# Performance work log

Measured on AMD Instinct MI355X. Metric: run time of the kernel, lower is better.

Reference implementation:

```python
import jax, jax.numpy as jnp
import numpy as np

B, N, D = 1, 4096, 3072
H, DH = 16, 64
INNER = H * DH  # 1024
SCALE = DH ** -0.5
EPS = 1e-5


def setup_inputs() -> dict:
    key = jax.random.key(0)
    ks = jax.random.split(key, 4)
    x = jax.random.normal(ks[0], (B, N, D), jnp.float32)
    pe = jax.random.normal(ks[1], (1, 1, N, DH // 2, 2, 2), jnp.float32)
    w_qkv = jax.random.normal(ks[2], (3 * INNER, D), jnp.float32) * 0.02
    w_out = jax.random.normal(ks[3], (D, INNER), jnp.float32) * 0.02
    ln_g = jnp.ones((D,), jnp.float32)
    ln_b = jnp.zeros((D,), jnp.float32)
    return {"x": x, "pe": pe, "w_qkv": w_qkv, "w_out": w_out, "ln_g": ln_g, "ln_b": ln_b}


def _apply_rope(t, pe):
    # t: [b,h,n,d], pe: [1,1,n,d/2,2,2] (Flux rope layout)
    b, h, n, d = t.shape
    t_ = t.reshape(b, h, n, d // 2, 1, 2)
    out = pe[..., 0] * t_[..., 0] + pe[..., 1] * t_[..., 1]  # [b,h,n,d/2,2]
    return out.reshape(b, h, n, d)


def reference(x, pe, w_qkv, w_out, ln_g, ln_b):
    # LayerNorm (norm2)
    mu = jnp.mean(x, axis=-1, keepdims=True)
    var = jnp.mean((x - mu) ** 2, axis=-1, keepdims=True)
    xn = (x - mu) / jnp.sqrt(var + EPS) * ln_g + ln_b
    # QKV projection (no bias)
    qkv = xn @ w_qkv.T  # [b,n,3*inner]
    q, k, v = jnp.split(qkv, 3, axis=-1)
    def split_heads(t):
        return t.reshape(B, N, H, DH).transpose(0, 2, 1, 3)  # b h n d
    q, k, v = split_heads(q), split_heads(k), split_heads(v)
    # RoPE on q and k (attention_aug_bbox with mask=None, aug idx = -1 -> plain rope attn)
    q = _apply_rope(q, pe)
    k = _apply_rope(k, pe)
    scores = jnp.einsum('bhqd,bhkd->bhqk', q, k) * SCALE
    attn = jax.nn.softmax(scores, axis=-1)
    o = jnp.einsum('bhqk,bhkd->bhqd', attn, v)
    o = o.transpose(0, 2, 1, 3).reshape(B, N, INNER)  # b n (h d)
    return o @ w_out.T  # [b,n,dim]
```

## Files before the change

kernel.cpp:

```cpp
#include <hip/hip_runtime.h>
#include <hip/hip_bf16.h>

typedef unsigned short u16;
typedef __attribute__((ext_vector_type(8))) short bf16x8;
typedef __attribute__((ext_vector_type(4))) float f32x4;

#define N_TOK 4096
#define DMODEL 3072
#define NH 16
#define DHEAD 64
#define INNER 1024
#define SCALE_LOG2E 0.18033688011112042f

__device__ __forceinline__ u16 f2bf(float f) {
    union { float f; unsigned u; } un; un.f = f;
    unsigned r = un.u + 0x7fffu + ((un.u >> 16) & 1u);
    return (u16)(r >> 16);
}
__device__ __forceinline__ float bf2f(u16 u) {
    union { unsigned u; float f; } x; x.u = ((unsigned)u) << 16; return x.f;
}
__device__ __forceinline__ unsigned pk2bf(float a, float b) {
    union { float f; unsigned u; } ua, ub; ua.f = a; ub.f = b;
    return __builtin_amdgcn_perm(ub.u + 0x8000u, ua.u + 0x8000u, 0x07060302u);
}
__device__ __forceinline__ void load_lds16(const u16* g, u16* l) {
    __builtin_amdgcn_global_load_lds(
        (const __attribute__((address_space(1))) unsigned int*)g,
        (__attribute__((address_space(3))) unsigned int*)l, 16, 0, 0);
}

__global__ __launch_bounds__(256) void ln_kernel(const float* __restrict__ x,
                                                 const float* __restrict__ g,
                                                 const float* __restrict__ b,
                                                 u16* __restrict__ xn) {
    int row = blockIdx.x;
    int tid = threadIdx.x;
    const float4* xr = (const float4*)(x + (size_t)row * DMODEL);
    float4 v[3];
    float s = 0.f, ss = 0.f;
#pragma unroll
    for (int i = 0; i < 3; ++i) {
        v[i] = xr[i * 256 + tid];
        s  += v[i].x + v[i].y + v[i].z + v[i].w;
        ss += v[i].x * v[i].x + v[i].y * v[i].y + v[i].z * v[i].z + v[i].w * v[i].w;
    }
#pragma unroll
    for (int off = 32; off; off >>= 1) {
        s  += __shfl_xor(s, off);
        ss += __shfl_xor(ss, off);
    }
    __shared__ float red[8];
    int wid = tid >> 6, lane = tid & 63;
    if (lane == 0) { red[wid] = s; red[wid + 4] = ss; }
    __syncthreads();
    s  = red[0] + red[1] + red[2] + red[3];
    ss = red[4] + red[5] + red[6] + red[7];
    float mean = s * (1.f / DMODEL);
    float var  = ss * (1.f / DMODEL) - mean * mean;
    float rstd = rsqrtf(var + 1e-5f);
    ushort4* orow = (ushort4*)(xn + (size_t)row * DMODEL);
#pragma unroll
    for (int i = 0; i < 3; ++i) {
        float4 gg = ((const float4*)g)[i * 256 + tid];
        float4 bb = ((const float4*)b)[i * 256 + tid];
        ushort4 o;
        o.x = f2bf((v[i].x - mean) * rstd * gg.x + bb.x);
        o.y = f2bf((v[i].y - mean) * rstd * gg.y + bb.y);
        o.z = f2bf((v[i].z - mean) * rstd * gg.z + bb.z);
        o.w = f2bf((v[i].w - mean) * rstd * gg.w + bb.w);
        orow[i * 256 + tid] = o;
    }
}

__global__ __launch_bounds__(256) void cvt_bf16(const float* __restrict__ in,
                                                u16* __restrict__ out, int n4) {
    int i = blockIdx.x * 256 + threadIdx.x;
    if (i < n4) {
        float4 v = ((const float4*)in)[i];
        ushort4 o;
        o.x = f2bf(v.x); o.y = f2bf(v.y); o.z = f2bf(v.z); o.w = f2bf(v.w);
        ((ushort4*)out)[i] = o;
    }
}

template <int CBF16>
__global__ __launch_bounds__(256) void gemm_bt(const u16* __restrict__ A,
                                               const u16* __restrict__ B,
                                               void* __restrict__ C,
                                               int M, int Nn, int K) {
    __shared__ u16 As[128 * 32];
    __shared__ u16 Bs[128 * 32];
    int tid = threadIdx.x;
    int lane = tid & 63, wid = tid >> 6;
    int wm = wid >> 1, wn = wid & 1;
    int l15 = lane & 15, quad = lane >> 4;
    int m0 = blockIdx.y * 128, n0 = blockIdx.x * 128;

    f32x4 zero4 = {0.f, 0.f, 0.f, 0.f};
    f32x4 acc[4][4];
#pragma unroll
    for (int i = 0; i < 4; ++i)
#pragma unroll
        for (int j = 0; j < 4; ++j) acc[i][j] = zero4;

    const u16* Ab = A + (size_t)m0 * K;
    const u16* Bb = B + (size_t)n0 * K;
    int row0 = tid >> 2, c0 = (((tid & 3) ^ ((lane >> 3) & 3)) * 8);
    int row1 = row0 + 64;
    int rsw = (l15 >> 1) & 3;

    for (int k0 = 0; k0 < K; k0 += 32) {
        load_lds16(Ab + (size_t)row0 * K + k0 + c0, &As[wid * 512]);
        load_lds16(Ab + (size_t)row1 * K + k0 + c0, &As[2048 + wid * 512]);
        load_lds16(Bb + (size_t)row0 * K + k0 + c0, &Bs[wid * 512]);
        load_lds16(Bb + (size_t)row1 * K + k0 + c0, &Bs[2048 + wid * 512]);
        __syncthreads();
        bf16x8 a[4], b[4];
#pragma unroll
        for (int t = 0; t < 4; ++t) {
            a[t] = *(const bf16x8*)&As[(wm * 64 + t * 16 + l15) * 32 + ((quad ^ rsw) * 8)];
            b[t] = *(const bf16x8*)&Bs[(wn * 64 + t * 16 + l15) * 32 + ((quad ^ rsw) * 8)];
        }
#pragma unroll
        for (int mt = 0; mt < 4; ++mt)
#pragma unroll
            for (int nt = 0; nt < 4; ++nt)
                acc[mt][nt] = __builtin_amdgcn_mfma_f32_16x16x32_bf16(a[mt], b[nt], acc[mt][nt], 0, 0, 0);
        __syncthreads();
    }
#pragma unroll
    for (int mt = 0; mt < 4; ++mt)
#pragma unroll
        for (int nt = 0; nt < 4; ++nt)
#pragma unroll
            for (int r = 0; r < 4; ++r) {
                int rr = m0 + wm * 64 + mt * 16 + quad * 4 + r;
                int cc = n0 + wn * 64 + nt * 16 + l15;
                if (CBF16)
                    ((u16*)C)[(size_t)rr * Nn + cc] = f2bf(acc[mt][nt][r]);
                else
                    ((float*)C)[(size_t)rr * Nn + cc] = acc[mt][nt][r];
            }
}

__global__ __launch_bounds__(256) void rope_qk(const u16* __restrict__ qkv,
                                               const float* __restrict__ pe,
                                               u16* __restrict__ Qr,
                                               u16* __restrict__ Kr) {
    int n = blockIdx.x;
    int tid = threadIdx.x;
    const u16* qrow = qkv + (size_t)n * DMODEL;
    const float4* pen = (const float4*)(pe + (size_t)n * 128);
#pragma unroll
    for (int it = 0; it < 2; ++it) {
        int p = it * 256 + tid;
        int h = p >> 5, i = p & 31;
        float4 w = pen[i];
        size_t obase = ((size_t)h * N_TOK + n) * DHEAD + 2 * i;
        unsigned qq = *(const unsigned*)&qrow[h * 64 + 2 * i];
        float q0 = bf2f((u16)qq), q1 = bf2f((u16)(qq >> 16));
        *(unsigned*)&Qr[obase] = pk2bf((w.x * q0 + w.y * q1) * SCALE_LOG2E,
                                       (w.z * q0 + w.w * q1) * SCALE_LOG2E);
        unsigned kk = *(const unsigned*)&qrow[INNER + h * 64 + 2 * i];
        float k0 = bf2f((u16)kk), k1 = bf2f((u16)(kk >> 16));
        *(unsigned*)&Kr[obase] = pk2bf(w.x * k0 + w.y * k1, w.z * k0 + w.w * k1);
    }
}

__global__ __launch_bounds__(256) void v_transpose(const u16* __restrict__ qkv,
                                                   u16* __restrict__ Vt) {
    __shared__ u16 t[64][65];
    int n0 = blockIdx.x * 64;
    int h = blockIdx.y;
    int tid = threadIdx.x;
#pragma unroll
    for (int it = 0; it < 4; ++it) {
        int nr = it * 16 + (tid >> 4);
        int dc = (tid & 15) * 4;
        ushort4 v = *(const ushort4*)&qkv[(size_t)(n0 + nr) * DMODEL + 2 * INNER + h * 64 + dc];
        t[dc + 0][nr] = v.x; t[dc + 1][nr] = v.y; t[dc + 2][nr] = v.z; t[dc + 3][nr] = v.w;
    }
    __syncthreads();
#pragma unroll
    for (int it = 0; it < 4; ++it) {
        int dr = it * 16 + (tid >> 4);
        int nc = (tid & 15) * 4;
        ushort4 v;
        v.x = t[dr][nc]; v.y = t[dr][nc + 1]; v.z = t[dr][nc + 2]; v.w = t[dr][nc + 3];
        *(ushort4*)&Vt[((size_t)h * 64 + dr) * N_TOK + n0 + nc] = v;
    }
}

__global__ __launch_bounds__(256, 2) void flash_attn(const u16* __restrict__ Q,
                                                     const u16* __restrict__ K,
                                                     const u16* __restrict__ Vt,
                                                     u16* __restrict__ O) {
    __shared__ u16 lds_all[16384];
    u16* Ks = lds_all;
    u16* Vs = lds_all + 4096;
    int tid = threadIdx.x, lane = tid & 63, wid = tid >> 6;
    u16* Ps = lds_all + 8192 + wid * 2048;
    int l15 = lane & 15, quad = lane >> 4;
    int sw = l15 & 7;
    int h = blockIdx.y;
    int q0 = blockIdx.x * 128 + wid * 32;
    const u16* Qh = Q + (size_t)h * N_TOK * DHEAD;
    const u16* Kh = K + (size_t)h * N_TOK * DHEAD;
    const u16* Vh = Vt + (size_t)h * DHEAD * N_TOK;

    f32x4 zero4 = {0.f, 0.f, 0.f, 0.f};
    bf16x8 ones;
#pragma unroll
    for (int i = 0; i < 8; ++i) ones[i] = (short)0x3F80;

    bf16x8 aq[2][2];
#pragma unroll
    for (int mtQ = 0; mtQ < 2; ++mtQ)
#pragma unroll
        for (int kc = 0; kc < 2; ++kc)
            aq[mtQ][kc] = *(const bf16x8*)&Qh[(size_t)(q0 + mtQ * 16 + l15) * DHEAD + kc * 32 + quad * 8];

    f32x4 o[2][4], lacc[2];
#pragma unroll
    for (int mtQ = 0; mtQ < 2; ++mtQ) {
#pragma unroll
        for (int dt = 0; dt < 4; ++dt) o[mtQ][dt] = zero4;
        lacc[mtQ] = zero4;
    }

    int rbase = wid * 16;
    int rowoff = lane >> 3;
    int csw = ((lane & 7) ^ rowoff) * 8;

    for (int kt = 0; kt < N_TOK; kt += 64) {
        load_lds16(&Kh[(size_t)(kt + rbase + rowoff) * DHEAD + csw], &Ks[rbase * 64]);
        load_lds16(&Kh[(size_t)(kt + rbase + 8 + rowoff) * DHEAD + csw], &Ks[(rbase + 8) * 64]);
        load_lds16(&Vh[(size_t)(rbase + rowoff) * N_TOK + kt + csw], &Vs[rbase * 64]);
        load_lds16(&Vh[(size_t)(rbase + 8 + rowoff) * N_TOK + kt + csw], &Vs[(rbase + 8) * 64]);
        __syncthreads();

        bf16x8 bk[4][2], av[4][2];
#pragma unroll
        for (int t = 0; t < 4; ++t)
#pragma unroll
            for (int kc = 0; kc < 2; ++kc) {
                int off = (t * 16 + l15) * 64 + (((kc * 4 + quad) ^ sw) * 8);
                bk[t][kc] = *(const bf16x8*)&Ks[off];
                av[t][kc] = *(const bf16x8*)&Vs[off];
            }
        __syncthreads();

#pragma unroll
        for (int mtQ = 0; mtQ < 2; ++mtQ) {
            f32x4 s[4];
#pragma unroll
            for (int ntK = 0; ntK < 4; ++ntK) {
                f32x4 t0 = __builtin_amdgcn_mfma_f32_16x16x32_bf16(bk[ntK][0], aq[mtQ][0], zero4, 0, 0, 0);
                s[ntK] = __builtin_amdgcn_mfma_f32_16x16x32_bf16(bk[ntK][1], aq[mtQ][1], t0, 0, 0, 0);
            }
#pragma unroll
            for (int ntK = 0; ntK < 4; ++ntK) {
                uint2 pv;
                pv.x = pk2bf(__builtin_amdgcn_exp2f(s[ntK][0]), __builtin_amdgcn_exp2f(s[ntK][1]));
                pv.y = pk2bf(__builtin_amdgcn_exp2f(s[ntK][2]), __builtin_amdgcn_exp2f(s[ntK][3]));
                int pc = (ntK * 2 + (quad >> 1)) ^ sw;
                *(uint2*)&Ps[(mtQ * 16 + l15) * 64 + pc * 8 + (quad & 1) * 4] = pv;
            }
            bf16x8 bp0 = *(const bf16x8*)&Ps[(mtQ * 16 + l15) * 64 + ((quad ^ sw) * 8)];
            bf16x8 bp1 = *(const bf16x8*)&Ps[(mtQ * 16 + l15) * 64 + (((4 + quad) ^ sw) * 8)];
            lacc[mtQ] = __builtin_amdgcn_mfma_f32_16x16x32_bf16(ones, bp0, lacc[mtQ], 0, 0, 0);
            lacc[mtQ] = __builtin_amdgcn_mfma_f32_16x16x32_bf16(ones, bp1, lacc[mtQ], 0, 0, 0);
#pragma unroll
            for (int dt = 0; dt < 4; ++dt) {
                o[mtQ][dt] = __builtin_amdgcn_mfma_f32_16x16x32_bf16(av[dt][0], bp0, o[mtQ][dt], 0, 0, 0);
                o[mtQ][dt] = __builtin_amdgcn_mfma_f32_16x16x32_bf16(av[dt][1], bp1, o[mtQ][dt], 0, 0, 0);
            }
        }
    }

    __syncthreads();
    u16* scratch = lds_all + wid * 2048;
#pragma unroll
    for (int mtQ = 0; mtQ < 2; ++mtQ) {
        float rl = 1.f / lacc[mtQ][0];
#pragma unroll
        for (int dt = 0; dt < 4; ++dt) {
            uint2 ov;
            ov.x = pk2bf(o[mtQ][dt][0] * rl, o[mtQ][dt][1] * rl);
            ov.y = pk2bf(o[mtQ][dt][2] * rl, o[mtQ][dt][3] * rl);
            *(uint2*)&scratch[(mtQ * 16 + l15) * 64 + dt * 16 + quad * 4] = ov;
        }
    }
#pragma unroll
    for (int p = 0; p < 4; ++p) {
        int q_local = p * 8 + (lane >> 3);
        int dcol = (lane & 7) * 8;
        bf16x8 v = *(const bf16x8*)&scratch[q_local * 64 + dcol];
        *(bf16x8*)&O[(size_t)(q0 + q_local) * INNER + h * 64 + dcol] = v;
    }
}

extern "C" void kernel_launch(void* const* d_in, const int* in_sizes, int n_in,
                              void* d_out, int out_size, void* d_ws, size_t ws_size,
                              hipStream_t stream) {
    const float* x     = (const float*)d_in[0];
    const float* pe    = (const float*)d_in[1];
    const float* w_qkv = (const float*)d_in[2];
    const float* w_out = (const float*)d_in[3];
    const float* ln_g  = (const float*)d_in[4];
    const float* ln_b  = (const float*)d_in[5];
    float* out = (float*)d_out;

    char* ws = (char*)d_ws;
    u16* xn  = (u16*)ws;  ws += (size_t)N_TOK * DMODEL * 2;
    u16* wq  = (u16*)ws;  ws += (size_t)3 * INNER * DMODEL * 2;
    u16* wo  = (u16*)ws;  ws += (size_t)DMODEL * INNER * 2;
    u16* qkv = (u16*)ws;  ws += (size_t)N_TOK * DMODEL * 2;
    u16* Qr  = (u16*)ws;  ws += (size_t)NH * N_TOK * DHEAD * 2;
    u16* Kr  = (u16*)ws;  ws += (size_t)NH * N_TOK * DHEAD * 2;
    u16* Vt  = (u16*)ws;  ws += (size_t)NH * DHEAD * N_TOK * 2;
    u16* Ob  = (u16*)ws;  ws += (size_t)N_TOK * INNER * 2;

    ln_kernel<<<N_TOK, 256, 0, stream>>>(x, ln_g, ln_b, xn);
    {
        int n4 = 3 * INNER * DMODEL / 4;
        cvt_bf16<<<(n4 + 255) / 256, 256, 0, stream>>>(w_qkv, wq, n4);
    }
    {
        int n4 = DMODEL * INNER / 4;
        cvt_bf16<<<(n4 + 255) / 256, 256, 0, stream>>>(w_out, wo, n4);
    }
    gemm_bt<1><<<dim3(DMODEL / 128, N_TOK / 128), 256, 0, stream>>>(xn, wq, qkv, N_TOK, DMODEL, DMODEL);
    rope_qk<<<N_TOK, 256, 0, stream>>>(qkv, pe, Qr, Kr);
    v_transpose<<<dim3(N_TOK / 64, NH), 256, 0, stream>>>(qkv, Vt);
    flash_attn<<<dim3(N_TOK / 128, NH), 256, 0, stream>>>(Qr, Kr, Vt, Ob);
    gemm_bt<0><<<dim3(DMODEL / 128, N_TOK / 128), 256, 0, stream>>>(Ob, wo, out, N_TOK, DMODEL, INNER);
}
```

Baseline: 400.5 us.

## Fuse RoPE and V transpose into QKV GEMM epilogue; merge prep kernels

The QKV GEMM now stages its output tile through LDS and, in the epilogue, applies RoPE and scaling to Q/K or writes V transposed directly. This removes the intermediate qkv buffer along with the separate rope and v_transpose kernels and their global round trips. LayerNorm and both weight conversions are merged into a single launch. The cost is a longer epilogue with extra LDS syncs, plus heavier pe reads spread across GEMM blocks.

```diff
diff --git a/kernel.cpp b/kernel.cpp
--- a/kernel.cpp
+++ b/kernel.cpp
@@ -24,18 +24,41 @@
     union { float f; unsigned u; } ua, ub; ua.f = a; ub.f = b;
     return __builtin_amdgcn_perm(ub.u + 0x8000u, ua.u + 0x8000u, 0x07060302u);
 }
+__device__ __forceinline__ unsigned mlo(unsigned a, unsigned b) {
+    return __builtin_amdgcn_perm(b, a, 0x05040100u);
+}
+__device__ __forceinline__ unsigned mhi(unsigned a, unsigned b) {
+    return __builtin_amdgcn_perm(b, a, 0x07060302u);
+}
 __device__ __forceinline__ void load_lds16(const u16* g, u16* l) {
     __builtin_amdgcn_global_load_lds(
         (const __attribute__((address_space(1))) unsigned int*)g,
         (__attribute__((address_space(3))) unsigned int*)l, 16, 0, 0);
 }
 
-__global__ __launch_bounds__(256) void ln_kernel(const float* __restrict__ x,
-                                                 const float* __restrict__ g,
-                                                 const float* __restrict__ b,
-                                                 u16* __restrict__ xn) {
-    int row = blockIdx.x;
+#define WQ_BLOCKS 9216
+#define WO_BLOCKS 3072
+__global__ __launch_bounds__(256) void prep(const float* __restrict__ x,
+                                            const float* __restrict__ g,
+                                            const float* __restrict__ b,
+                                            u16* __restrict__ xn,
+                                            const float* __restrict__ w_qkv,
+                                            u16* __restrict__ wq,
+                                            const float* __restrict__ w_out,
+                                            u16* __restrict__ wo) {
+    int blk = blockIdx.x;
     int tid = threadIdx.x;
+    if (blk >= N_TOK) {
+        const float* src; u16* dst; int i;
+        if (blk < N_TOK + WQ_BLOCKS) { src = w_qkv; dst = wq; i = (blk - N_TOK) * 256 + tid; }
+        else { src = w_out; dst = wo; i = (blk - N_TOK - WQ_BLOCKS) * 256 + tid; }
+        float4 v = ((const float4*)src)[i];
+        ushort4 o;
+        o.x = f2bf(v.x); o.y = f2bf(v.y); o.z = f2bf(v.z); o.w = f2bf(v.w);
+        ((ushort4*)dst)[i] = o;
+        return;
+    }
+    int row = blk;
     const float4* xr = (const float4*)(x + (size_t)row * DMODEL);
     float4 v[3];
     float s = 0.f, ss = 0.f;
@@ -73,14 +96,126 @@
     }
 }
 
-__global__ __launch_bounds__(256) void cvt_bf16(const float* __restrict__ in,
-                                                u16* __restrict__ out, int n4) {
-    int i = blockIdx.x * 256 + threadIdx.x;
-    if (i < n4) {
-        float4 v = ((const float4*)in)[i];
-        ushort4 o;
-        o.x = f2bf(v.x); o.y = f2bf(v.y); o.z = f2bf(v.z); o.w = f2bf(v.w);
-        ((ushort4*)out)[i] = o;
+__global__ __launch_bounds__(256) void gemm_qkv(const u16* __restrict__ A,
+                                                const u16* __restrict__ B,
+                                                const float* __restrict__ pe,
+                                                u16* __restrict__ Qr,
+                                                u16* __restrict__ Kr,
+                                                u16* __restrict__ Vt) {
+    __shared__ u16 sbuf[8704];
+    u16* As = sbuf;
+    u16* Bs = sbuf + 4096;
+    int tid = threadIdx.x;
+    int lane = tid & 63, wid = tid >> 6;
+    int wm = wid >> 1, wn = wid & 1;
+    int l15 = lane & 15, quad = lane >> 4;
+    int m0 = blockIdx.y * 128, n0 = blockIdx.x * 128;
+    const int K = DMODEL;
+
+    f32x4 zero4 = {0.f, 0.f, 0.f, 0.f};
+    f32x4 acc[4][4];
+#pragma unroll
+    for (int i = 0; i < 4; ++i)
+#pragma unroll
+        for (int j = 0; j < 4; ++j) acc[i][j] = zero4;
+
+    const u16* Ab = A + (size_t)m0 * K;
+    const u16* Bb = B + (size_t)n0 * K;
+    int row0 = tid >> 2, c0 = (((tid & 3) ^ ((lane >> 3) & 3)) * 8);
+    int row1 = row0 + 64;
+    int rsw = (l15 >> 1) & 3;
+
+    for (int k0 = 0; k0 < K; k0 += 32) {
+        load_lds16(Ab + (size_t)row0 * K + k0 + c0, &As[wid * 512]);
+        load_lds16(Ab + (size_t)row1 * K + k0 + c0, &As[2048 + wid * 512]);
+        load_lds16(Bb + (size_t)row0 * K + k0 + c0, &Bs[wid * 512]);
+        load_lds16(Bb + (size_t)row1 * K + k0 + c0, &Bs[2048 + wid * 512]);
+        __syncthreads();
+        bf16x8 a[4], b[4];
+#pragma unroll
+        for (int t = 0; t < 4; ++t) {
+            a[t] = *(const bf16x8*)&As[(wm * 64 + t * 16 + l15) * 32 + ((quad ^ rsw) * 8)];
+            b[t] = *(const bf16x8*)&Bs[(wn * 64 + t * 16 + l15) * 32 + ((quad ^ rsw) * 8)];
+        }
+#pragma unroll
+        for (int mt = 0; mt < 4; ++mt)
+#pragma unroll
+            for (int nt = 0; nt < 4; ++nt)
+                acc[mt][nt] = __builtin_amdgcn_mfma_f32_16x16x32_bf16(a[mt], b[nt], acc[mt][nt], 0, 0, 0);
+        __syncthreads();
+    }
+
+    u16* tile = sbuf;
+    int region = n0 >> 10;
+    int n0l = n0 & 1023;
+
+#pragma unroll
+    for (int p = 0; p < 2; ++p) {
+        if (p) __syncthreads();
+        if (wm == p) {
+#pragma unroll
+            for (int mt = 0; mt < 4; ++mt)
+#pragma unroll
+                for (int nt = 0; nt < 4; ++nt)
+#pragma unroll
+                    for (int r = 0; r < 4; ++r)
+                        tile[(mt * 16 + quad * 4 + r) * 136 + wn * 64 + nt * 16 + l15] =
+                            f2bf(acc[mt][nt][r]);
+        }
+        __syncthreads();
+
+        if (region < 2) {
+            int rl = tid >> 2;
+            int ch = (tid & 3) * 32;
+            int n  = m0 + p * 64 + rl;
+            int cg = n0l + ch;
+            int h  = cg >> 6;
+            int dbase = cg & 63;
+            float sc = (region == 0) ? SCALE_LOG2E : 1.0f;
+            u16* outb = (region == 0) ? Qr : Kr;
+            const float4* pev = (const float4*)pe + (size_t)n * 32 + (dbase >> 1);
+            u16* orow = outb + ((size_t)h * N_TOK + n) * DHEAD + dbase;
+#pragma unroll
+            for (int k = 0; k < 4; ++k) {
+                uint4 td = *(const uint4*)&tile[rl * 136 + ch + k * 8];
+                float4 w0 = pev[k * 4 + 0];
+                float4 w1 = pev[k * 4 + 1];
+                float4 w2 = pev[k * 4 + 2];
+                float4 w3 = pev[k * 4 + 3];
+                float a0 = bf2f((u16)td.x), b0 = bf2f((u16)(td.x >> 16));
+                float a1 = bf2f((u16)td.y), b1 = bf2f((u16)(td.y >> 16));
+                float a2 = bf2f((u16)td.z), b2 = bf2f((u16)(td.z >> 16));
+                float a3 = bf2f((u16)td.w), b3 = bf2f((u16)(td.w >> 16));
+                uint4 ov;
+                ov.x = pk2bf((w0.x * a0 + w0.y * b0) * sc, (w0.z * a0 + w0.w * b0) * sc);
+                ov.y = pk2bf((w1.x * a1 + w1.y * b1) * sc, (w1.z * a1 + w1.w * b1) * sc);
+                ov.z = pk2bf((w2.x * a2 + w2.y * b2) * sc, (w2.z * a2 + w2.w * b2) * sc);
+                ov.w = pk2bf((w3.x * a3 + w3.y * b3) * sc, (w3.z * a3 + w3.w * b3) * sc);
+                *(uint4*)&orow[k * 8] = ov;
+            }
+        } else {
+            int c  = (tid & 63) * 2;
+            int rq = (wid) * 16;
+            int cg = n0l + c;
+            int h = cg >> 6, d = cg & 63;
+            int nb = m0 + p * 64 + rq;
+            u16* vrow0 = Vt + ((size_t)(h * 64 + d)) * N_TOK + nb;
+            u16* vrow1 = vrow0 + N_TOK;
+            unsigned lo[8], hi[8];
+#pragma unroll
+            for (int k = 0; k < 4; ++k) {
+                unsigned v0 = *(const unsigned*)&tile[(rq + 4 * k + 0) * 136 + c];
+                unsigned v1 = *(const unsigned*)&tile[(rq + 4 * k + 1) * 136 + c];
+                unsigned v2 = *(const unsigned*)&tile[(rq + 4 * k + 2) * 136 + c];
+                unsigned v3 = *(const unsigned*)&tile[(rq + 4 * k + 3) * 136 + c];
+                lo[2 * k] = mlo(v0, v1); lo[2 * k + 1] = mlo(v2, v3);
+                hi[2 * k] = mhi(v0, v1); hi[2 * k + 1] = mhi(v2, v3);
+            }
+            ((uint4*)vrow0)[0] = *(uint4*)&lo[0];
+            ((uint4*)vrow0)[1] = *(uint4*)&lo[4];
+            ((uint4*)vrow1)[0] = *(uint4*)&hi[0];
+            ((uint4*)vrow1)[1] = *(uint4*)&hi[4];
+        }
     }
 }
 
@@ -142,54 +277,6 @@
                 else
                     ((float*)C)[(size_t)rr * Nn + cc] = acc[mt][nt][r];
             }
-}
-
-__global__ __launch_bounds__(256) void rope_qk(const u16* __restrict__ qkv,
-                                               const float* __restrict__ pe,
-                                               u16* __restrict__ Qr,
-                                               u16* __restrict__ Kr) {
-    int n = blockIdx.x;
-    int tid = threadIdx.x;
-    const u16* qrow = qkv + (size_t)n * DMODEL;
-    const float4* pen = (const float4*)(pe + (size_t)n * 128);
-#pragma unroll
-    for (int it = 0; it < 2; ++it) {
-        int p = it * 256 + tid;
-        int h = p >> 5, i = p & 31;
-        float4 w = pen[i];
-        size_t obase = ((size_t)h * N_TOK + n) * DHEAD + 2 * i;
-        unsigned qq = *(const unsigned*)&qrow[h * 64 + 2 * i];
-        float q0 = bf2f((u16)qq), q1 = bf2f((u16)(qq >> 16));
-        *(unsigned*)&Qr[obase] = pk2bf((w.x * q0 + w.y * q1) * SCALE_LOG2E,
-                                       (w.z * q0 + w.w * q1) * SCALE_LOG2E);
-        unsigned kk = *(const unsigned*)&qrow[INNER + h * 64 + 2 * i];
-        float k0 = bf2f((u16)kk), k1 = bf2f((u16)(kk >> 16));
-        *(unsigned*)&Kr[obase] = pk2bf(w.x * k0 + w.y * k1, w.z * k0 + w.w * k1);
-    }
-}
-
-__global__ __launch_bounds__(256) void v_transpose(const u16* __restrict__ qkv,
-                                                   u16* __restrict__ Vt) {
-    __shared__ u16 t[64][65];
-    int n0 = blockIdx.x * 64;
-    int h = blockIdx.y;
-    int tid = threadIdx.x;
-#pragma unroll
-    for (int it = 0; it < 4; ++it) {
-        int nr = it * 16 + (tid >> 4);
-        int dc = (tid & 15) * 4;
-        ushort4 v = *(const ushort4*)&qkv[(size_t)(n0 + nr) * DMODEL + 2 * INNER + h * 64 + dc];
-        t[dc + 0][nr] = v.x; t[dc + 1][nr] = v.y; t[dc + 2][nr] = v.z; t[dc + 3][nr] = v.w;
-    }
-    __syncthreads();
-#pragma unroll
-    for (int it = 0; it < 4; ++it) {
-        int dr = it * 16 + (tid >> 4);
-        int nc = (tid & 15) * 4;
-        ushort4 v;
-        v.x = t[dr][nc]; v.y = t[dr][nc + 1]; v.z = t[dr][nc + 2]; v.w = t[dr][nc + 3];
-        *(ushort4*)&Vt[((size_t)h * 64 + dr) * N_TOK + n0 + nc] = v;
-    }
 }
 
 __global__ __launch_bounds__(256, 2) void flash_attn(const u16* __restrict__ Q,
@@ -316,24 +403,13 @@
     u16* xn  = (u16*)ws;  ws += (size_t)N_TOK * DMODEL * 2;
     u16* wq  = (u16*)ws;  ws += (size_t)3 * INNER * DMODEL * 2;
     u16* wo  = (u16*)ws;  ws += (size_t)DMODEL * INNER * 2;
-    u16* qkv = (u16*)ws;  ws += (size_t)N_TOK * DMODEL * 2;
     u16* Qr  = (u16*)ws;  ws += (size_t)NH * N_TOK * DHEAD * 2;
     u16* Kr  = (u16*)ws;  ws += (size_t)NH * N_TOK * DHEAD * 2;
     u16* Vt  = (u16*)ws;  ws += (size_t)NH * DHEAD * N_TOK * 2;
     u16* Ob  = (u16*)ws;  ws += (size_t)N_TOK * INNER * 2;
 
-    ln_kernel<<<N_TOK, 256, 0, stream>>>(x, ln_g, ln_b, xn);
-    {
-        int n4 = 3 * INNER * DMODEL / 4;
-        cvt_bf16<<<(n4 + 255) / 256, 256, 0, stream>>>(w_qkv, wq, n4);
-    }
-    {
-        int n4 = DMODEL * INNER / 4;
-        cvt_bf16<<<(n4 + 255) / 256, 256, 0, stream>>>(w_out, wo, n4);
-    }
-    gemm_bt<1><<<dim3(DMODEL / 128, N_TOK / 128), 256, 0, stream>>>(xn, wq, qkv, N_TOK, DMODEL, DMODEL);
-    rope_qk<<<N_TOK, 256, 0, stream>>>(qkv, pe, Qr, Kr);
-    v_transpose<<<dim3(N_TOK / 64, NH), 256, 0, stream>>>(qkv, Vt);
+    prep<<<N_TOK + WQ_BLOCKS + WO_BLOCKS, 256, 0, stream>>>(x, ln_g, ln_b, xn, w_qkv, wq, w_out, wo);
+    gemm_qkv<<<dim3(DMODEL / 128, N_TOK / 128), 256, 0, stream>>>(xn, wq, pe, Qr, Kr, Vt);
     flash_attn<<<dim3(N_TOK / 128, NH), 256, 0, stream>>>(Qr, Kr, Vt, Ob);
     gemm_bt<0><<<dim3(DMODEL / 128, N_TOK / 128), 256, 0, stream>>>(Ob, wo, out, N_TOK, DMODEL, INNER);
 }
```

Result: slower. 458.5 us (+14.5%).
